# Kernel optimization log

Measured on AMD Instinct MI355X. Metric: run time of the kernel, lower is better.

## Reference

```python
import jax, jax.numpy as jnp
import numpy as np

FEATURE_DIM = 128
N_NODES = 100000
N_EDGES = 800000
L1_IN = 2 * FEATURE_DIM            # 256
L1_OUT = int((2 * FEATURE_DIM) ** 0.5)  # 16
L2_DIM = L1_OUT + 1                # 17


def leaky(x):
    return jnp.where(x >= 0, x, 0.1 * x)


def setup_inputs() -> dict:
    key = jax.random.key(0)
    ks = jax.random.split(key, 8)
    Jt_ind = jax.random.randint(ks[0], (2, N_EDGES), 0, N_NODES)
    Jt_val = jax.random.normal(ks[1], (N_EDGES,), dtype=jnp.float32)
    f = jax.random.normal(ks[2], (N_NODES, FEATURE_DIM), dtype=jnp.float32)
    W1 = jax.random.normal(ks[3], (L1_IN, L1_OUT), dtype=jnp.float32) * (1.0 / np.sqrt(L1_IN))
    b1 = jnp.zeros((L1_OUT,), dtype=jnp.float32)
    W2 = jax.random.normal(ks[4], (L2_DIM, L2_DIM), dtype=jnp.float32) * (1.0 / np.sqrt(L2_DIM))
    b2 = jnp.zeros((L2_DIM,), dtype=jnp.float32)
    Wc = jax.random.normal(ks[5], (L2_DIM, 1), dtype=jnp.float32) * (1.0 / np.sqrt(L2_DIM))
    bc = jnp.ones((1,), dtype=jnp.float32)  # collapse_bias = 1
    return {"Jt_ind": Jt_ind, "Jt_val": Jt_val, "f": f, "N": N_NODES,
            "W1": W1, "b1": b1, "W2": W2, "b2": b2, "Wc": Wc, "bc": bc}


def reference(Jt_ind, Jt_val, f, N, W1, b1, W2, b2, Wc, bc):
    i = Jt_ind[0]
    j = Jt_ind[1]
    absv = jnp.abs(Jt_val)                                     # [E]
    # degree: per-destination sum of |Jt_val|
    deg_abs = jax.ops.segment_sum(absv, i, num_segments=N)     # [N]
    Jt_val_abs_norm = absv / deg_abs[i]                        # [E]
    # gather endpoint features and run tiny edge-MLP
    x = jnp.concatenate([f[i], f[j]], axis=1)                  # [E, 2F]
    x = leaky(x @ W1 + b1)                                     # [E, L1_OUT]
    x = jnp.concatenate([x, Jt_val_abs_norm[:, None]], axis=1) # [E, L2_DIM]
    x = leaky(x @ W2 + b2)                                     # [E, L2_DIM]
    e_values = (x @ Wc + bc)[:, 0]                             # [E]
    # segment softmax over edges grouped by destination i (stable)
    m = jax.ops.segment_max(e_values, i, num_segments=N)       # [N]
    ex = jnp.exp(e_values - m[i])                              # [E]
    s = jax.ops.segment_sum(ex, i, num_segments=N)             # [N]
    return ex / s[i]                                           # [E]
```

## Files before the change

kernel.cpp:

```cpp
#include <hip/hip_runtime.h>
#include <hip/hip_fp16.h>
#include <math.h>

#define FDIM  128
#define L1OUT 16
#define L2DIM 17
#define TR    64
#define TSTR  129

struct __align__(16) H16 { __half2 h[8]; };

__device__ __forceinline__ float lrelu(float v) { return v >= 0.f ? v : 0.1f * v; }

__global__ void node_transform(const float* __restrict__ f,
                               const float* __restrict__ W1,
                               H16* __restrict__ A, H16* __restrict__ B,
                               float* __restrict__ deg, float* __restrict__ ssum,
                               int N) {
    __shared__ float tile[TR * TSTR];
    __shared__ float w1s[256 * L1OUT];

    int t   = threadIdx.x;
    int gid = blockIdx.x * 256 + t;
    if (gid < N) { deg[gid] = 0.f; ssum[gid] = 0.f; }

    {
        const float4* src = reinterpret_cast<const float4*>(W1);
        float4*       dst = reinterpret_cast<float4*>(w1s);
#pragma unroll
        for (int q = 0; q < 4; ++q) dst[t + 256 * q] = src[t + 256 * q];
    }
    int base = blockIdx.x * TR;
#pragma unroll
    for (int q = 0; q < 8; ++q) {
        int i4 = t + 256 * q;
        int r  = i4 >> 5;
        int c4 = i4 & 31;
        float4 v = make_float4(0.f, 0.f, 0.f, 0.f);
        if (base + r < N)
            v = reinterpret_cast<const float4*>(f + (size_t)(base + r) * FDIM)[c4];
        float* d = &tile[r * TSTR + c4 * 4];
        d[0] = v.x; d[1] = v.y; d[2] = v.z; d[3] = v.w;
    }
    __syncthreads();

    int lane    = t & 63;
    int w       = t >> 6;
    int colbase = (w & 1) * 8;
    int krowoff = (w >> 1) * FDIM;

    float acc[8];
#pragma unroll
    for (int c = 0; c < 8; ++c) acc[c] = 0.f;

    const float* trow  = &tile[lane * TSTR];
    const float* wbase = &w1s[krowoff * L1OUT + colbase];
#pragma unroll 4
    for (int k = 0; k < FDIM; ++k) {
        float x = trow[k];
        const float4* wr = reinterpret_cast<const float4*>(wbase + k * L1OUT);
        float4 w0 = wr[0], w1v = wr[1];
        acc[0] += x * w0.x;  acc[1] += x * w0.y;
        acc[2] += x * w0.z;  acc[3] += x * w0.w;
        acc[4] += x * w1v.x; acc[5] += x * w1v.y;
        acc[6] += x * w1v.z; acc[7] += x * w1v.w;
    }

    int n = base + lane;
    if (n < N) {
        __half2 h[4];
#pragma unroll
        for (int q = 0; q < 4; ++q)
            h[q] = __floats2half2_rn(acc[2 * q], acc[2 * q + 1]);
        H16* arr = (w >> 1) ? B : A;
        float4* dst = reinterpret_cast<float4*>(
            reinterpret_cast<char*>(arr + n) + (w & 1) * 16);
        *dst = *reinterpret_cast<float4*>(h);
    }
}

__global__ void deg_accum(const int* __restrict__ ind_i, const float* __restrict__ val,
                          float* __restrict__ deg, int E) {
    int t = blockIdx.x * blockDim.x + threadIdx.x;
    int e = t * 4;
    if (e + 3 < E) {
        int4   ii = *reinterpret_cast<const int4*>(ind_i + e);
        float4 vv = *reinterpret_cast<const float4*>(val + e);
        atomicAdd(&deg[ii.x], fabsf(vv.x));
        atomicAdd(&deg[ii.y], fabsf(vv.y));
        atomicAdd(&deg[ii.z], fabsf(vv.z));
        atomicAdd(&deg[ii.w], fabsf(vv.w));
    } else {
        for (; e < E; ++e) atomicAdd(&deg[ind_i[e]], fabsf(val[e]));
    }
}

__global__ void edge_mlp(const int* __restrict__ ind, const float* __restrict__ val,
                         const H16* __restrict__ A, const H16* __restrict__ B,
                         const float* __restrict__ deg,
                         const float* __restrict__ b1,
                         const float* __restrict__ W2, const float* __restrict__ b2,
                         const float* __restrict__ Wc, const float* __restrict__ bc,
                         float* __restrict__ eout, float* __restrict__ ssum, int E) {
    __shared__ float w2s[L2DIM * 20];
    __shared__ float b1s[L1OUT];
    __shared__ float b2s[L2DIM];
    __shared__ float wcs[L2DIM];
    __shared__ float bc0s;

    int t = threadIdx.x;
    for (int idx = t; idx < L2DIM * L2DIM; idx += 256) {
        int c = idx / L2DIM, r = idx % L2DIM;
        w2s[c * 20 + r] = W2[idx];
    }
    if (t < L1OUT) b1s[t] = b1[t];
    if (t < L2DIM) b2s[t] = b2[t];
    if (t < L2DIM) wcs[t] = Wc[t];
    if (t == 0)    bc0s   = bc[0];
    __syncthreads();

    int e = blockIdx.x * 256 + t;
    if (e >= E) return;

    int i = ind[e];
    int j = ind[E + e];
    H16 a  = A[i];
    H16 bb = B[j];
    float v  = val[e];
    float dg = deg[i];

    float x[L2DIM];
#pragma unroll
    for (int q = 0; q < 8; ++q) {
        float2 fa = __half22float2(a.h[q]);
        float2 fb = __half22float2(bb.h[q]);
        x[2 * q]     = lrelu(fa.x + fb.x + b1s[2 * q]);
        x[2 * q + 1] = lrelu(fa.y + fb.y + b1s[2 * q + 1]);
    }
    x[L1OUT] = fabsf(v) / dg;

    float acc[L2DIM];
#pragma unroll
    for (int r = 0; r < L2DIM; ++r) acc[r] = b2s[r];
#pragma unroll
    for (int c = 0; c < L2DIM; ++c) {
        float xc = x[c];
        const float4* r4 = reinterpret_cast<const float4*>(&w2s[c * 20]);
        float4 w0 = r4[0], w1 = r4[1], w2v = r4[2], w3 = r4[3];
        float  w16 = w2s[c * 20 + 16];
        acc[0]  += xc * w0.x;  acc[1]  += xc * w0.y;
        acc[2]  += xc * w0.z;  acc[3]  += xc * w0.w;
        acc[4]  += xc * w1.x;  acc[5]  += xc * w1.y;
        acc[6]  += xc * w1.z;  acc[7]  += xc * w1.w;
        acc[8]  += xc * w2v.x; acc[9]  += xc * w2v.y;
        acc[10] += xc * w2v.z; acc[11] += xc * w2v.w;
        acc[12] += xc * w3.x;  acc[13] += xc * w3.y;
        acc[14] += xc * w3.z;  acc[15] += xc * w3.w;
        acc[16] += xc * w16;
    }
    float ev = bc0s;
#pragma unroll
    for (int r = 0; r < L2DIM; ++r) ev += lrelu(acc[r]) * wcs[r];

    float ex = __expf(ev);
    eout[e] = ex;
    atomicAdd(&ssum[i], ex);
}

__global__ void normalize(const int* __restrict__ ind_i, const float* __restrict__ ssum,
                          float* __restrict__ ex, int E) {
    int t = blockIdx.x * blockDim.x + threadIdx.x;
    int e = t * 4;
    if (e + 3 < E) {
        int4   ii = *reinterpret_cast<const int4*>(ind_i + e);
        float4 vv = *reinterpret_cast<const float4*>(ex + e);
        vv.x /= ssum[ii.x];
        vv.y /= ssum[ii.y];
        vv.z /= ssum[ii.z];
        vv.w /= ssum[ii.w];
        *reinterpret_cast<float4*>(ex + e) = vv;
    } else {
        for (; e < E; ++e) ex[e] = ex[e] / ssum[ind_i[e]];
    }
}

extern "C" void kernel_launch(void* const* d_in, const int* in_sizes, int n_in,
                              void* d_out, int out_size, void* d_ws, size_t ws_size,
                              hipStream_t stream) {
    const int*   Jt_ind = (const int*)  d_in[0];
    const float* Jt_val = (const float*)d_in[1];
    const float* f      = (const float*)d_in[2];
    const float* W1 = (const float*)d_in[4];
    const float* b1 = (const float*)d_in[5];
    const float* W2 = (const float*)d_in[6];
    const float* b2 = (const float*)d_in[7];
    const float* Wc = (const float*)d_in[8];
    const float* bc = (const float*)d_in[9];

    const int E = in_sizes[1];
    const int N = in_sizes[2] / FDIM;
    float* out = (float*)d_out;

    char* ws = (char*)d_ws;
    H16*   A    = (H16*)ws;    ws += (size_t)N * sizeof(H16);
    H16*   Bm   = (H16*)ws;    ws += (size_t)N * sizeof(H16);
    float* deg  = (float*)ws;  ws += (size_t)N * sizeof(float);
    float* ssum = (float*)ws;  ws += (size_t)N * sizeof(float);

    const int B256 = 256;
    const int nblk = (N + TR - 1) / TR;
    const int eblk = (E + B256 - 1) / B256;
    const int qblk = ((E + 3) / 4 + B256 - 1) / B256;

    node_transform<<<nblk, B256, 0, stream>>>(f, W1, A, Bm, deg, ssum, N);
    deg_accum     <<<qblk, B256, 0, stream>>>(Jt_ind, Jt_val, deg, E);
    edge_mlp      <<<eblk, B256, 0, stream>>>(Jt_ind, Jt_val, A, Bm, deg,
                                              b1, W2, b2, Wc, bc, out, ssum, E);
    normalize     <<<qblk, B256, 0, stream>>>(Jt_ind, ssum, out, E);
}
```

Measured before the change: 232.9 us.

## Fuse four kernels into one persistent cooperative kernel with grid syncs

Replaces the four separate launches (node transform, degree accumulation, edge MLP, normalization) with one cooperative persistent kernel that loops over work with grid-stride loops and separates phases with grid.sync(). Degree accumulation now runs in the same phase right after the node transform, and the edge loop prefetches the next edge's indices. W1 is read from global memory instead of being staged in shared memory. The aim is to remove launch gaps, at the cost of grid-wide barriers and per-CU occupancy limits.

Result: slower. 621.1 us (+166.7%).

```diff
diff --git a/kernel.cpp b/kernel.cpp
--- a/kernel.cpp
+++ b/kernel.cpp
@@ -1,4 +1,5 @@
 #include <hip/hip_runtime.h>
+#include <hip/hip_cooperative_groups.h>
 #include <hip/hip_fp16.h>
 #include <math.h>
 
@@ -8,179 +9,188 @@
 #define TR    64
 #define TSTR  129
 
+namespace cg = cooperative_groups;
+
 struct __align__(16) H16 { __half2 h[8]; };
 
 __device__ __forceinline__ float lrelu(float v) { return v >= 0.f ? v : 0.1f * v; }
 
-__global__ void node_transform(const float* __restrict__ f,
-                               const float* __restrict__ W1,
-                               H16* __restrict__ A, H16* __restrict__ B,
-                               float* __restrict__ deg, float* __restrict__ ssum,
-                               int N) {
-    __shared__ float tile[TR * TSTR];
-    __shared__ float w1s[256 * L1OUT];
-
-    int t   = threadIdx.x;
-    int gid = blockIdx.x * 256 + t;
-    if (gid < N) { deg[gid] = 0.f; ssum[gid] = 0.f; }
-
-    {
-        const float4* src = reinterpret_cast<const float4*>(W1);
-        float4*       dst = reinterpret_cast<float4*>(w1s);
-#pragma unroll
-        for (int q = 0; q < 4; ++q) dst[t + 256 * q] = src[t + 256 * q];
-    }
-    int base = blockIdx.x * TR;
-#pragma unroll
-    for (int q = 0; q < 8; ++q) {
-        int i4 = t + 256 * q;
-        int r  = i4 >> 5;
-        int c4 = i4 & 31;
-        float4 v = make_float4(0.f, 0.f, 0.f, 0.f);
-        if (base + r < N)
-            v = reinterpret_cast<const float4*>(f + (size_t)(base + r) * FDIM)[c4];
-        float* d = &tile[r * TSTR + c4 * 4];
-        d[0] = v.x; d[1] = v.y; d[2] = v.z; d[3] = v.w;
-    }
-    __syncthreads();
-
-    int lane    = t & 63;
-    int w       = t >> 6;
-    int colbase = (w & 1) * 8;
-    int krowoff = (w >> 1) * FDIM;
-
-    float acc[8];
-#pragma unroll
-    for (int c = 0; c < 8; ++c) acc[c] = 0.f;
-
-    const float* trow  = &tile[lane * TSTR];
-    const float* wbase = &w1s[krowoff * L1OUT + colbase];
+__global__ __launch_bounds__(256, 4) void fused_gat(
+    const int* __restrict__ ind, const float* __restrict__ val,
+    const float* __restrict__ f, const float* __restrict__ W1,
+    const float* __restrict__ b1, const float* __restrict__ W2,
+    const float* __restrict__ b2, const float* __restrict__ Wc,
+    const float* __restrict__ bc, float* __restrict__ out,
+    H16* __restrict__ A, H16* __restrict__ Bm,
+    float* __restrict__ deg, float* __restrict__ ssum,
+    int N, int E)
+{
+    cg::grid_group grid = cg::this_grid();
+    __shared__ __align__(16) float smem[TR * TSTR];
+
+    const int t    = threadIdx.x;
+    const int gtid = blockIdx.x * 256 + t;
+    const int GT   = gridDim.x * 256;
+
+    for (int n = gtid; n < N; n += GT) { deg[n] = 0.f; ssum[n] = 0.f; }
+    grid.sync();
+
+    {
+        const int ntiles  = (N + TR - 1) / TR;
+        const int lane    = t & 63;
+        const int w       = t >> 6;
+        const int colbase = (w & 1) * 8;
+        const int krowoff = (w >> 1) * FDIM;
+        const float* wbase = W1 + (size_t)krowoff * L1OUT + colbase;
+
+        for (int tb = blockIdx.x; tb < ntiles; tb += gridDim.x) {
+            const int base = tb * TR;
+#pragma unroll
+            for (int q = 0; q < 8; ++q) {
+                int i4 = t + 256 * q;
+                int r  = i4 >> 5;
+                int c4 = i4 & 31;
+                float4 v = make_float4(0.f, 0.f, 0.f, 0.f);
+                if (base + r < N)
+                    v = reinterpret_cast<const float4*>(f + (size_t)(base + r) * FDIM)[c4];
+                float* d = &smem[r * TSTR + c4 * 4];
+                d[0] = v.x; d[1] = v.y; d[2] = v.z; d[3] = v.w;
+            }
+            __syncthreads();
+
+            float acc[8];
+#pragma unroll
+            for (int c = 0; c < 8; ++c) acc[c] = 0.f;
+            const float* trow = &smem[lane * TSTR];
 #pragma unroll 4
-    for (int k = 0; k < FDIM; ++k) {
-        float x = trow[k];
-        const float4* wr = reinterpret_cast<const float4*>(wbase + k * L1OUT);
-        float4 w0 = wr[0], w1v = wr[1];
-        acc[0] += x * w0.x;  acc[1] += x * w0.y;
-        acc[2] += x * w0.z;  acc[3] += x * w0.w;
-        acc[4] += x * w1v.x; acc[5] += x * w1v.y;
-        acc[6] += x * w1v.z; acc[7] += x * w1v.w;
-    }
-
-    int n = base + lane;
-    if (n < N) {
-        __half2 h[4];
-#pragma unroll
-        for (int q = 0; q < 4; ++q)
-            h[q] = __floats2half2_rn(acc[2 * q], acc[2 * q + 1]);
-        H16* arr = (w >> 1) ? B : A;
-        float4* dst = reinterpret_cast<float4*>(
-            reinterpret_cast<char*>(arr + n) + (w & 1) * 16);
-        *dst = *reinterpret_cast<float4*>(h);
-    }
-}
-
-__global__ void deg_accum(const int* __restrict__ ind_i, const float* __restrict__ val,
-                          float* __restrict__ deg, int E) {
-    int t = blockIdx.x * blockDim.x + threadIdx.x;
-    int e = t * 4;
-    if (e + 3 < E) {
-        int4   ii = *reinterpret_cast<const int4*>(ind_i + e);
-        float4 vv = *reinterpret_cast<const float4*>(val + e);
-        atomicAdd(&deg[ii.x], fabsf(vv.x));
-        atomicAdd(&deg[ii.y], fabsf(vv.y));
-        atomicAdd(&deg[ii.z], fabsf(vv.z));
-        atomicAdd(&deg[ii.w], fabsf(vv.w));
-    } else {
-        for (; e < E; ++e) atomicAdd(&deg[ind_i[e]], fabsf(val[e]));
-    }
-}
-
-__global__ void edge_mlp(const int* __restrict__ ind, const float* __restrict__ val,
-                         const H16* __restrict__ A, const H16* __restrict__ B,
-                         const float* __restrict__ deg,
-                         const float* __restrict__ b1,
-                         const float* __restrict__ W2, const float* __restrict__ b2,
-                         const float* __restrict__ Wc, const float* __restrict__ bc,
-                         float* __restrict__ eout, float* __restrict__ ssum, int E) {
-    __shared__ float w2s[L2DIM * 20];
-    __shared__ float b1s[L1OUT];
-    __shared__ float b2s[L2DIM];
-    __shared__ float wcs[L2DIM];
-    __shared__ float bc0s;
-
-    int t = threadIdx.x;
+            for (int k = 0; k < FDIM; ++k) {
+                float x = trow[k];
+                float4 w0  = *reinterpret_cast<const float4*>(wbase + (size_t)k * L1OUT);
+                float4 w1v = *reinterpret_cast<const float4*>(wbase + (size_t)k * L1OUT + 4);
+                acc[0] += x * w0.x;  acc[1] += x * w0.y;
+                acc[2] += x * w0.z;  acc[3] += x * w0.w;
+                acc[4] += x * w1v.x; acc[5] += x * w1v.y;
+                acc[6] += x * w1v.z; acc[7] += x * w1v.w;
+            }
+            int n = base + lane;
+            if (n < N) {
+                __align__(16) __half2 h[4];
+#pragma unroll
+                for (int q = 0; q < 4; ++q)
+                    h[q] = __floats2half2_rn(acc[2 * q], acc[2 * q + 1]);
+                H16* arr = (w >> 1) ? Bm : A;
+                float4* dst = reinterpret_cast<float4*>(
+                    reinterpret_cast<char*>(arr + n) + (w & 1) * 16);
+                *dst = *reinterpret_cast<float4*>(h);
+            }
+            __syncthreads();
+        }
+    }
+
+    {
+        const int E4 = E >> 2;
+        for (int q = gtid; q < E4; q += GT) {
+            int e = q << 2;
+            int4   ii = *reinterpret_cast<const int4*>(ind + e);
+            float4 vv = *reinterpret_cast<const float4*>(val + e);
+            atomicAdd(&deg[ii.x], fabsf(vv.x));
+            atomicAdd(&deg[ii.y], fabsf(vv.y));
+            atomicAdd(&deg[ii.z], fabsf(vv.z));
+            atomicAdd(&deg[ii.w], fabsf(vv.w));
+        }
+        if (gtid < (E & 3)) {
+            int e = (E & ~3) + gtid;
+            atomicAdd(&deg[ind[e]], fabsf(val[e]));
+        }
+    }
+
+    float* w2s = smem;
+    float* b1s = smem + L2DIM * 20;
+    float* b2s = b1s + L1OUT;
+    float* wcs = b2s + L2DIM;
+    float* bcs = wcs + L2DIM;
     for (int idx = t; idx < L2DIM * L2DIM; idx += 256) {
-        int c = idx / L2DIM, r = idx % L2DIM;
+        int c = idx / L2DIM, r = idx - c * L2DIM;
         w2s[c * 20 + r] = W2[idx];
     }
     if (t < L1OUT) b1s[t] = b1[t];
     if (t < L2DIM) b2s[t] = b2[t];
     if (t < L2DIM) wcs[t] = Wc[t];
-    if (t == 0)    bc0s   = bc[0];
-    __syncthreads();
-
-    int e = blockIdx.x * 256 + t;
-    if (e >= E) return;
-
-    int i = ind[e];
-    int j = ind[E + e];
-    H16 a  = A[i];
-    H16 bb = B[j];
-    float v  = val[e];
-    float dg = deg[i];
-
-    float x[L2DIM];
-#pragma unroll
-    for (int q = 0; q < 8; ++q) {
-        float2 fa = __half22float2(a.h[q]);
-        float2 fb = __half22float2(bb.h[q]);
-        x[2 * q]     = lrelu(fa.x + fb.x + b1s[2 * q]);
-        x[2 * q + 1] = lrelu(fa.y + fb.y + b1s[2 * q + 1]);
-    }
-    x[L1OUT] = fabsf(v) / dg;
-
-    float acc[L2DIM];
-#pragma unroll
-    for (int r = 0; r < L2DIM; ++r) acc[r] = b2s[r];
-#pragma unroll
-    for (int c = 0; c < L2DIM; ++c) {
-        float xc = x[c];
-        const float4* r4 = reinterpret_cast<const float4*>(&w2s[c * 20]);
-        float4 w0 = r4[0], w1 = r4[1], w2v = r4[2], w3 = r4[3];
-        float  w16 = w2s[c * 20 + 16];
-        acc[0]  += xc * w0.x;  acc[1]  += xc * w0.y;
-        acc[2]  += xc * w0.z;  acc[3]  += xc * w0.w;
-        acc[4]  += xc * w1.x;  acc[5]  += xc * w1.y;
-        acc[6]  += xc * w1.z;  acc[7]  += xc * w1.w;
-        acc[8]  += xc * w2v.x; acc[9]  += xc * w2v.y;
-        acc[10] += xc * w2v.z; acc[11] += xc * w2v.w;
-        acc[12] += xc * w3.x;  acc[13] += xc * w3.y;
-        acc[14] += xc * w3.z;  acc[15] += xc * w3.w;
-        acc[16] += xc * w16;
-    }
-    float ev = bc0s;
-#pragma unroll
-    for (int r = 0; r < L2DIM; ++r) ev += lrelu(acc[r]) * wcs[r];
-
-    float ex = __expf(ev);
-    eout[e] = ex;
-    atomicAdd(&ssum[i], ex);
-}
-
-__global__ void normalize(const int* __restrict__ ind_i, const float* __restrict__ ssum,
-                          float* __restrict__ ex, int E) {
-    int t = blockIdx.x * blockDim.x + threadIdx.x;
-    int e = t * 4;
-    if (e + 3 < E) {
-        int4   ii = *reinterpret_cast<const int4*>(ind_i + e);
-        float4 vv = *reinterpret_cast<const float4*>(ex + e);
-        vv.x /= ssum[ii.x];
-        vv.y /= ssum[ii.y];
-        vv.z /= ssum[ii.z];
-        vv.w /= ssum[ii.w];
-        *reinterpret_cast<float4*>(ex + e) = vv;
-    } else {
-        for (; e < E; ++e) ex[e] = ex[e] / ssum[ind_i[e]];
+    if (t == 0)    bcs[0] = bc[0];
+    grid.sync();
+
+    {
+        int  e     = gtid;
+        bool valid = e < E;
+        int  i_c = 0, j_c = 0; float v_c = 0.f;
+        if (valid) { i_c = ind[e]; j_c = ind[E + e]; v_c = val[e]; }
+
+        while (valid) {
+            H16  a  = A[i_c];
+            H16  bb = Bm[j_c];
+            float dg = deg[i_c];
+
+            int  e_n = e + GT;
+            bool vn  = e_n < E;
+            int  i_n = 0, j_n = 0; float v_n = 0.f;
+            if (vn) { i_n = ind[e_n]; j_n = ind[E + e_n]; v_n = val[e_n]; }
+
+            float x[L2DIM];
+#pragma unroll
+            for (int q = 0; q < 8; ++q) {
+                float2 fa = __half22float2(a.h[q]);
+                float2 fb = __half22float2(bb.h[q]);
+                x[2 * q]     = lrelu(fa.x + fb.x + b1s[2 * q]);
+                x[2 * q + 1] = lrelu(fa.y + fb.y + b1s[2 * q + 1]);
+            }
+            x[L1OUT] = fabsf(v_c) / dg;
+
+            float acc[L2DIM];
+#pragma unroll
+            for (int r = 0; r < L2DIM; ++r) acc[r] = b2s[r];
+#pragma unroll
+            for (int c = 0; c < L2DIM; ++c) {
+                float xc = x[c];
+                const float4* r4 = reinterpret_cast<const float4*>(&w2s[c * 20]);
+                float4 w0 = r4[0], w1v = r4[1], w2v = r4[2], w3 = r4[3];
+                float  w16 = w2s[c * 20 + 16];
+                acc[0]  += xc * w0.x;  acc[1]  += xc * w0.y;
+                acc[2]  += xc * w0.z;  acc[3]  += xc * w0.w;
+                acc[4]  += xc * w1v.x; acc[5]  += xc * w1v.y;
+                acc[6]  += xc * w1v.z; acc[7]  += xc * w1v.w;
+                acc[8]  += xc * w2v.x; acc[9]  += xc * w2v.y;
+                acc[10] += xc * w2v.z; acc[11] += xc * w2v.w;
+                acc[12] += xc * w3.x;  acc[13] += xc * w3.y;
+                acc[14] += xc * w3.z;  acc[15] += xc * w3.w;
+                acc[16] += xc * w16;
+            }
+            float ev = bcs[0];
+#pragma unroll
+            for (int r = 0; r < L2DIM; ++r) ev += lrelu(acc[r]) * wcs[r];
+
+            float ex = __expf(ev);
+            out[e] = ex;
+            atomicAdd(&ssum[i_c], ex);
+
+            e = e_n; i_c = i_n; j_c = j_n; v_c = v_n; valid = vn;
+        }
+    }
+    grid.sync();
+
+    {
+        const int E4 = E >> 2;
+        for (int q = gtid; q < E4; q += GT) {
+            int e = q << 2;
+            int4   ii = *reinterpret_cast<const int4*>(ind + e);
+            float4 vv = *reinterpret_cast<const float4*>(out + e);
+            vv.x /= ssum[ii.x]; vv.y /= ssum[ii.y];
+            vv.z /= ssum[ii.z]; vv.w /= ssum[ii.w];
+            *reinterpret_cast<float4*>(out + e) = vv;
+        }
+        if (gtid < (E & 3)) {
+            int e = (E & ~3) + gtid;
+            out[e] = out[e] / ssum[ind[e]];
+        }
     }
 }
 
@@ -197,8 +207,8 @@
     const float* Wc = (const float*)d_in[8];
     const float* bc = (const float*)d_in[9];
 
-    const int E = in_sizes[1];
-    const int N = in_sizes[2] / FDIM;
+    int E = in_sizes[1];
+    int N = in_sizes[2] / FDIM;
     float* out = (float*)d_out;
 
     char* ws = (char*)d_ws;
@@ -207,14 +217,19 @@
     float* deg  = (float*)ws;  ws += (size_t)N * sizeof(float);
     float* ssum = (float*)ws;  ws += (size_t)N * sizeof(float);
 
-    const int B256 = 256;
-    const int nblk = (N + TR - 1) / TR;
-    const int eblk = (E + B256 - 1) / B256;
-    const int qblk = ((E + 3) / 4 + B256 - 1) / B256;
-
-    node_transform<<<nblk, B256, 0, stream>>>(f, W1, A, Bm, deg, ssum, N);
-    deg_accum     <<<qblk, B256, 0, stream>>>(Jt_ind, Jt_val, deg, E);
-    edge_mlp      <<<eblk, B256, 0, stream>>>(Jt_ind, Jt_val, A, Bm, deg,
-                                              b1, W2, b2, Wc, bc, out, ssum, E);
-    normalize     <<<qblk, B256, 0, stream>>>(Jt_ind, ssum, out, E);
+    int dev = 0;
+    hipGetDevice(&dev);
+    int numCU = 256;
+    hipDeviceGetAttribute(&numCU, hipDeviceAttributeMultiprocessorCount, dev);
+    int blocksPerCU = 0;
+    hipOccupancyMaxActiveBlocksPerMultiprocessor(&blocksPerCU, fused_gat, 256, 0);
+    if (blocksPerCU < 1) blocksPerCU = 1;
+    int grid = blocksPerCU * numCU;
+
+    void* args[] = { (void*)&Jt_ind, (void*)&Jt_val, (void*)&f, (void*)&W1,
+                     (void*)&b1, (void*)&W2, (void*)&b2, (void*)&Wc, (void*)&bc,
+                     (void*)&out, (void*)&A, (void*)&Bm, (void*)&deg, (void*)&ssum,
+                     (void*)&N, (void*)&E };
+    hipLaunchCooperativeKernel(reinterpret_cast<void*>(fused_gat),
+                               dim3(grid), dim3(256), args, 0, stream);
 }
```
